# Kernel tuning notes

Hardware: AMD Instinct MI355X
Metric: run time of the kernel (lower is better)

The kernel has to match this reference:

```python
import jax, jax.numpy as jnp
import numpy as np

B, G, S, GS, P = 32, 512, 128, 32, 10
C, H, RED = 384, 6, 16
HID = 4 * C
D = C // H
SCALE = D ** -0.5

def _gelu(x):
    return jax.nn.gelu(x, approximate=False)

def _ln(x, g, b):
    m = jnp.mean(x, -1, keepdims=True)
    v = jnp.var(x, -1, keepdims=True)
    return (x - m) * jax.lax.rsqrt(v + 1e-5) * g + b

def _split_qkv(x, W):
    Bn, T, Cc = x.shape
    qkv = (x @ W).reshape(Bn, T, 3, H, D).transpose(2, 0, 3, 1, 4)
    return qkv[0], qkv[1], qkv[2]

def _merge(x):
    Bn, Hh, T, Dd = x.shape
    return x.transpose(0, 2, 1, 3).reshape(Bn, T, Hh * Dd)

def _mha(q, k, v):
    a = jax.nn.softmax(jnp.einsum('bhnd,bhmd->bhnm', q, k) * SCALE, axis=-1)
    return jnp.einsum('bhnm,bhmd->bhnd', a, v)

def _forward(x, center1, center2, neighborhood, prompt_embeddings, ln1_g, ln1_b, Wqkv, Wproj, bproj, gate, ln2_g, ln2_b, W1, b1, W2, b2, ad_down_W, ad_down_b, ad_up_W, ad_up_b, ad_gate, bn_g, bn_b, bn_mean, bn_var, ln3_g, ln3_b, a1_Wqkv, a1_Wproj, a1_bproj, ad1_down_W, ad1_down_b, ad1_up_W, ad1_up_b, idx, center_idx, group_size, if_maxmean, pro_cof, center_cof):
    Bx, Ntok, Cc = x.shape
    # prompt dropout is identity in eval
    prompt = jnp.broadcast_to(prompt_embeddings, (Bx, P, Cc))
    # --- gated dual self / prompt-cross attention ---
    xn = _ln(x, ln1_g, ln1_b)
    q, k, v = _split_qkv(xn, Wqkv)
    xs = _mha(q, k, v)                                  # [B,H,N,D]
    _, pk, pv = _split_qkv(prompt, Wqkv)
    pa = jax.nn.softmax(jnp.einsum('bhnd,bhpd->bhnp', q, pk) * SCALE, axis=-1)
    px = jnp.einsum('bhnp,bhpd->bhnd', gate * pa, pv)   # learned gate per head
    x = x + (_merge(xs) + _merge(px)) @ Wproj + bproj
    # --- MLP + gated bottleneck adapter residual ---
    h = _gelu(_ln(x, ln2_g, ln2_b) @ W1 + b1) @ W2 + b2
    h_ad = h + _gelu(h @ ad_down_W + ad_down_b) @ ad_up_W + ad_up_b
    x = ad_gate * h_ad + x
    cls_x = x[:, :1]
    xt = x[:, 1:]                                       # [B,G,C]
    flat = xt.reshape(Bx * G, Cc)
    x_nb = flat[idx].reshape(Bx * S, group_size, Cc)    # KNN neighborhoods
    x_ct = flat[center_idx].reshape(Bx, S, Cc)          # center features
    # NOTE: original normalizes `neighborhood` by its std, but result is unused
    # --- local self-attention (attn1 over norm3) on each neighborhood ---
    nq, nk, nv = _split_qkv(_ln(x_nb, ln3_g, ln3_b), a1_Wqkv)
    no = _mha(nq, nk, nv)
    x_nb = x_nb + _merge(no) @ a1_Wproj + a1_bproj
    knn = x_nb.reshape(Bx, S, group_size, Cc)
    lc = jnp.max(knn, axis=2)
    if if_maxmean:
        lc = lc + jnp.mean(knn, axis=2)
    # BatchNorm1d (eval, running stats) + GELU over channel dim
    lc = _gelu((lc - bn_mean) * jax.lax.rsqrt(bn_var + 1e-5) * bn_g + bn_b)
    vis = lc + center_cof * x_ct                        # [B,S,C]
    # --- propagate: de_neighbors == S so sorted-topk == full weighted sum ---
    d = jnp.sum((center1[:, :, None, :] - center2[:, None, :, :]) ** 2, axis=-1)  # [B,G,S]
    w = 1.0 / (d + 1e-8)
    w = w / jnp.sum(w, axis=-1, keepdims=True)
    interp = jnp.einsum('bns,bsc->bnc', w, vis)
    xt = xt + pro_cof * interp
    out = jnp.concatenate([cls_x, xt], axis=1)
    # adapter1
    out = out + _gelu(out @ ad1_down_W + ad1_down_b) @ ad1_up_W + ad1_up_b
    return out

def setup_inputs():
    ks = jax.random.split(jax.random.key(0), 20)
    r = lambda i, shape, s=0.02: jax.random.normal(ks[i], shape, jnp.float32) * s
    return {
        'x': jax.random.normal(ks[0], (B, G + 1, C), jnp.float32),
        'center1': jax.random.normal(ks[1], (B, G, 3), jnp.float32),
        'center2': jax.random.normal(ks[2], (B, S, 3), jnp.float32),
        'neighborhood': jax.random.normal(ks[3], (B, S, GS, 3), jnp.float32),
        'prompt_embeddings': r(4, (P, C)),
        'ln1_g': jnp.ones(C), 'ln1_b': jnp.zeros(C),
        'Wqkv': r(5, (C, 3 * C)),
        'Wproj': r(6, (C, C)), 'bproj': jnp.zeros(C),
        'gate': jax.random.normal(ks[7], (1, H, 1, 1), jnp.float32),
        'ln2_g': jnp.ones(C), 'ln2_b': jnp.zeros(C),
        'W1': r(8, (C, HID)), 'b1': jnp.zeros(HID),
        'W2': r(9, (HID, C)), 'b2': jnp.zeros(C),
        'ad_down_W': r(10, (C, RED)), 'ad_down_b': jnp.zeros(RED),
        'ad_up_W': r(11, (RED, C)), 'ad_up_b': jnp.zeros(C),
        'ad_gate': jax.random.normal(ks[12], (), jnp.float32),
        'bn_g': jnp.ones(C), 'bn_b': jnp.zeros(C),
        'bn_mean': jnp.zeros(C), 'bn_var': jnp.ones(C),
        'ln3_g': jnp.ones(C), 'ln3_b': jnp.zeros(C),
        'a1_Wqkv': r(13, (C, 3 * C)),
        'a1_Wproj': r(14, (C, C)), 'a1_bproj': jnp.zeros(C),
        'ad1_down_W': r(15, (C, RED)), 'ad1_down_b': jnp.zeros(RED),
        'ad1_up_W': r(16, (RED, C)), 'ad1_up_b': jnp.zeros(C),
        'idx': jax.random.randint(ks[17], (B * S * GS,), 0, B * G),
        'center_idx': jax.random.randint(ks[18], (B * S,), 0, B * G),
        'group_size': GS,
        'if_maxmean': 1,
        'pro_cof': 1,
        'center_cof': 1,
    }

def reference(x, center1, center2, neighborhood, prompt_embeddings, ln1_g, ln1_b, Wqkv, Wproj, bproj, gate, ln2_g, ln2_b, W1, b1, W2, b2, ad_down_W, ad_down_b, ad_up_W, ad_up_b, ad_gate, bn_g, bn_b, bn_mean, bn_var, ln3_g, ln3_b, a1_Wqkv, a1_Wproj, a1_bproj, ad1_down_W, ad1_down_b, ad1_up_W, ad1_up_b, idx, center_idx, group_size, if_maxmean, pro_cof, center_cof):
    return _forward(x, center1, center2, neighborhood, prompt_embeddings, ln1_g, ln1_b, Wqkv, Wproj, bproj, gate, ln2_g, ln2_b, W1, b1, W2, b2, ad_down_W, ad_down_b, ad_up_W, ad_up_b, ad_gate, bn_g, bn_b, bn_mean, bn_var, ln3_g, ln3_b, a1_Wqkv, a1_Wproj, a1_bproj, ad1_down_W, ad1_down_b, ad1_up_W, ad1_up_b, idx, center_idx, group_size, if_maxmean, pro_cof, center_cof)
```

## Files before the change

### kernel.cpp

```cpp
#include <hip/hip_runtime.h>
#include <hip/hip_bf16.h>
#include <cstdint>
#include <cstddef>

typedef __hip_bfloat16 bf16;
constexpr int TOK = 32 * 513;

typedef __attribute__((ext_vector_type(8))) short short8;
typedef __attribute__((ext_vector_type(4))) float f32x4;

__device__ __forceinline__ float bflo(unsigned u){ return __uint_as_float(u << 16); }
__device__ __forceinline__ float bfhi(unsigned u){ return __uint_as_float(u & 0xffff0000u); }
__device__ __forceinline__ float b2f(bf16 x){ return __bfloat162float(x); }
__device__ __forceinline__ bf16  f2b(float x){ return __float2bfloat16(x); }
__device__ __forceinline__ float geluf(float x){ return 0.5f*x*(1.0f + erff(x*0.70710678118654752f)); }
__device__ __forceinline__ void unp8(uint4 u, float* f){
  f[0]=bflo(u.x); f[1]=bfhi(u.x); f[2]=bflo(u.y); f[3]=bfhi(u.y);
  f[4]=bflo(u.z); f[5]=bfhi(u.z); f[6]=bflo(u.w); f[7]=bfhi(u.w);
}
__device__ __forceinline__ float scal(const int* p){
  const int i = *p;
  if (i > -1000000 && i < 1000000) return (float)i;
  return __int_as_float(i);
}
__device__ __forceinline__ f32x4 mfma16(short8 a, short8 b, f32x4 c){
  return __builtin_amdgcn_mfma_f32_16x16x32_bf16(a, b, c, 0, 0, 0);
}
__device__ __forceinline__ int swzl(int l){ return l ^ ((l >> 3) & 7); }

__global__ __launch_bounds__(256) void detect_kernel(const unsigned* __restrict__ x,
                                                     int* __restrict__ flag)
{
  const int t = threadIdx.x;
  bool bad = false;
  for (int i = t; i < 2048; i += 256){
    const unsigned u = x[i];
    const float a = fabsf(bflo(u)), b = fabsf(bfhi(u));
    if (!(a < 1e6f) || !(b < 1e6f)) bad = true;
  }
  __shared__ int s;
  if (t == 0) s = 0;
  __syncthreads();
  const unsigned long long m = __ballot(bad);
  if (m != 0ull && (t & 63) == 0) atomicOr(&s, 1);
  __syncthreads();
  if (t == 0) *flag = s;
}

struct ConvArgs {
  const void* src[34];
  bf16*       dst[34];
  int         n[34];
};
__global__ __launch_bounds__(256) void convert_many(const int* __restrict__ flag, ConvArgs a)
{
  const int ii = blockIdx.y;
  const bool isf = (*flag != 0);
  const int n = a.n[ii];
  const int n8 = n >> 3;
  bf16* d = a.dst[ii];
  if (isf){
    const float4* s = (const float4*)a.src[ii];
    for (int i = blockIdx.x*256 + threadIdx.x; i < n8; i += gridDim.x*256){
      const float4 f0 = s[i*2];
      const float4 f1 = s[i*2 + 1];
      bf16 tmp[8] = {f2b(f0.x),f2b(f0.y),f2b(f0.z),f2b(f0.w),
                     f2b(f1.x),f2b(f1.y),f2b(f1.z),f2b(f1.w)};
      *(uint4*)(d + (size_t)i*8) = *(const uint4*)tmp;
    }
  } else {
    const uint4* s = (const uint4*)a.src[ii];
    for (int i = blockIdx.x*256 + threadIdx.x; i < n8; i += gridDim.x*256){
      ((uint4*)d)[i] = s[i];
    }
  }
  if (blockIdx.x == 0){
    for (int i = n8*8 + threadIdx.x; i < n; i += 256){
      d[i] = isf ? f2b(((const float*)a.src[ii])[i]) : ((const bf16*)a.src[ii])[i];
    }
  }
}

__global__ __launch_bounds__(256) void shuffle_b(const bf16* __restrict__ W,
    bf16* __restrict__ out, int N, int KT, int NT)
{
  const int id = blockIdx.x*256 + threadIdx.x;
  if (id >= NT*KT*64) return;
  const int l  = id & 63;
  const int k0 = (id >> 6) % KT;
  const int n0 = (id >> 6) / KT;
  bf16 tmp[8];
  #pragma unroll
  for (int j = 0; j < 8; j++)
    tmp[j] = W[(size_t)(k0*32 + (l>>4)*8 + j)*N + n0*16 + (l&15)];
  *(uint4*)(out + (size_t)id*8) = *(const uint4*)tmp;
}

template<bool SRC_BF16>
__global__ __launch_bounds__(256) void ln_kernel(const void* __restrict__ src,
    const bf16* __restrict__ g, const bf16* __restrict__ b,
    bf16* __restrict__ out, int rows)
{
  const int wave = (blockIdx.x * blockDim.x + threadIdx.x) >> 6;
  const int lane = threadIdx.x & 63;
  if (wave >= rows) return;
  float v[6]; float s = 0.f, s2 = 0.f;
  #pragma unroll
  for (int i = 0; i < 6; i++){
    const int c = lane + 64*i;
    float x;
    if (SRC_BF16) x = b2f(((const bf16*)src)[(size_t)wave*384 + c]);
    else          x = ((const float*)src)[(size_t)wave*384 + c];
    v[i] = x; s += x; s2 += x*x;
  }
  #pragma unroll
  for (int mm = 32; mm; mm >>= 1){ s += __shfl_xor(s, mm); s2 += __shfl_xor(s2, mm); }
  const float mean = s * (1.f/384.f);
  const float rs = rsqrtf(s2 * (1.f/384.f) - mean*mean + 1e-5f);
  #pragma unroll
  for (int i = 0; i < 6; i++){
    const int c = lane + 64*i;
    out[(size_t)wave*384 + c] = f2b((v[i]-mean)*rs*b2f(g[c]) + b2f(b[c]));
  }
}

__global__ __launch_bounds__(256) void ln3_kernel(const float* __restrict__ xres,
    const bf16* __restrict__ g, const bf16* __restrict__ b, bf16* __restrict__ out)
{
  const int r = (blockIdx.x * blockDim.x + threadIdx.x) >> 6;
  const int lane = threadIdx.x & 63;
  if (r >= 16384) return;
  const int tok = (r >> 9)*513 + 1 + (r & 511);
  const float* xp = xres + (size_t)tok*384;
  float v[6]; float s = 0.f, s2 = 0.f;
  #pragma unroll
  for (int i = 0; i < 6; i++){
    const float x = xp[lane + 64*i];
    v[i] = x; s += x; s2 += x*x;
  }
  #pragma unroll
  for (int mm = 32; mm; mm >>= 1){ s += __shfl_xor(s, mm); s2 += __shfl_xor(s2, mm); }
  const float mean = s * (1.f/384.f);
  const float rs = rsqrtf(s2 * (1.f/384.f) - mean*mean + 1e-5f);
  #pragma unroll
  for (int i = 0; i < 6; i++){
    const int c = lane + 64*i;
    out[(size_t)r*384 + c] = f2b((v[i]-mean)*rs*b2f(g[c]) + b2f(b[c]));
  }
}

template<int EPI>
__global__ __launch_bounds__(256) void mfma_gemm(
    const bf16* __restrict__ A, const bf16* __restrict__ Bsh,
    const bf16* __restrict__ bias, const bf16* __restrict__ resid,
    void* __restrict__ outv, int M, int N, int K)
{
  __shared__ __align__(16) bf16 sA[8*64*8];
  const int t = threadIdx.x, lane = t & 63, w = t >> 6;
  const int l15 = lane & 15, quad = lane >> 4;
  const int wm = w & 1, wn = w >> 1;
  const int m0 = blockIdx.y * 128;
  const int n0t = blockIdx.x * 8 + wn * 4;
  const int KT = K >> 5;
  f32x4 acc[4][4];
  #pragma unroll
  for (int i = 0; i < 4; i++){
    #pragma unroll
    for (int j = 0; j < 4; j++) acc[i][j] = f32x4{0.f,0.f,0.f,0.f};
  }
  const int arow = t >> 1, ac0 = (t & 1) * 16;
  const int amt = arow >> 4, al15 = arow & 15, aq0 = (ac0 >> 3);

  for (int ks = 0; ks < KT; ks++){
    uint4 u0 = {0,0,0,0}, u1 = {0,0,0,0};
    const int gm = m0 + arow;
    if (gm < M){
      const bf16* ap = A + (size_t)gm*K + ks*32 + ac0;
      u0 = *(const uint4*)ap; u1 = *(const uint4*)(ap + 8);
    }
    *(uint4*)(sA + ((amt*64 + aq0*16     + al15) << 3)) = u0;
    *(uint4*)(sA + ((amt*64 + (aq0+1)*16 + al15) << 3)) = u1;
    __syncthreads();
    short8 afr[4];
    #pragma unroll
    for (int i = 0; i < 4; i++)
      afr[i] = *(const short8*)(sA + (((wm*4+i)*64 + lane) << 3));
    #pragma unroll
    for (int j = 0; j < 4; j++){
      const short8 b = *(const short8*)(Bsh + ((size_t)((n0t+j)*KT + ks)*64 + lane)*8);
      #pragma unroll
      for (int i = 0; i < 4; i++) acc[i][j] = mfma16(afr[i], b, acc[i][j]);
    }
    __syncthreads();
  }
  #pragma unroll
  for (int i = 0; i < 4; i++){
    #pragma unroll
    for (int r = 0; r < 4; r++){
      const int gm = m0 + (wm*4+i)*16 + quad*4 + r;
      if (gm < M){
        #pragma unroll
        for (int j = 0; j < 4; j++){
          const int gn = (n0t+j)*16 + l15;
          float v = acc[i][j][r];
          const size_t o = (size_t)gm*N + gn;
          if (EPI == 0){ v += b2f(bias[gn]); ((bf16*)outv)[o] = f2b(v); }
          else if (EPI == 1){ ((bf16*)outv)[o] = f2b(v); }
          else if (EPI == 2){ v += b2f(bias[gn]); ((bf16*)outv)[o] = f2b(geluf(v)); }
          else { v += b2f(bias[gn]) + b2f(resid[o]); ((float*)outv)[o] = v; }
        }
      }
    }
  }
}

__global__ __launch_bounds__(256) void pqkv_kernel(const bf16* __restrict__ pe,
    const bf16* __restrict__ Wqkv, float* __restrict__ pq)
{
  const int n  = blockIdx.x*64 + (threadIdx.x & 63);
  const int rg = threadIdx.x >> 6;
  for (int r = rg; r < 10; r += 4){
    float s0 = 0.f, s1 = 0.f;
    for (int c = 0; c < 384; c += 2){
      s0 = fmaf(b2f(pe[(size_t)r*384+c]),   b2f(Wqkv[(size_t)c*1152 + n]),     s0);
      s1 = fmaf(b2f(pe[(size_t)r*384+c+1]), b2f(Wqkv[(size_t)(c+1)*1152 + n]), s1);
    }
    pq[(size_t)r*1152 + n] = s0 + s1;
  }
}

__global__ __launch_bounds__(256) void attn_kernel(
    const bf16* __restrict__ qkv, const float* __restrict__ pq,
    const bf16* __restrict__ gate, bf16* __restrict__ ao)
{
  __shared__ __align__(16) bf16 s_q[64*72];
  __shared__ __align__(16) bf16 s_k[64*72];
  __shared__ __align__(16) bf16 s_vT[64*72];
  __shared__ __align__(16) bf16 s_p[4*16*40];
  __shared__ __align__(16) bf16 s_pk[16*72];
  __shared__ __align__(16) bf16 s_pvT[64*40];
  const int bh = blockIdx.y;
  const int b = bh / 6, h = bh % 6;
  const int q0 = blockIdx.x * 64;
  const int t = threadIdx.x, lane = t & 63, w = t >> 6;
  const int l15 = lane & 15, quad = lane >> 4;

  {
    const int row = t >> 2, dc = (t & 3) * 16;
    const int tok = q0 + row;
    uint4 u0 = {0,0,0,0}, u1 = {0,0,0,0};
    if (tok < 513){
      const bf16* p = qkv + (size_t)(b*513 + tok)*1152 + h*64 + dc;
      u0 = *(const uint4*)p; u1 = *(const uint4*)(p + 8);
    }
    *(uint4*)(s_q + row*72 + dc)     = u0;
    *(uint4*)(s_q + row*72 + dc + 8) = u1;
  }
  {
    const int j = t >> 4, dc = (t & 15) * 4;
    float f[4] = {0.f,0.f,0.f,0.f};
    if (j < 10){
      const float* pk = pq + (size_t)j*1152 + 384 + h*64 + dc;
      f[0]=pk[0]; f[1]=pk[1]; f[2]=pk[2]; f[3]=pk[3];
    }
    bf16 tmp[4] = {f2b(f[0]),f2b(f[1]),f2b(f[2]),f2b(f[3])};
    *(uint2*)(s_pk + j*72 + dc) = *(const uint2*)tmp;
  }
  {
    const int d = t & 63, kg = t >> 6;
    #pragma unroll
    for (int kk = 0; kk < 8; kk++){
      const int key = kg*8 + kk;
      bf16 v = f2b(0.f);
      if (key < 10) v = f2b(pq[(size_t)key*1152 + 768 + h*64 + d]);
      s_pvT[d*40 + key] = v;
    }
  }

  float m_i[4], l_i[4];
  f32x4 oacc[4];
  #pragma unroll
  for (int r = 0; r < 4; r++){ m_i[r] = -30000.f; l_i[r] = 0.f; }
  #pragma unroll
  for (int nt = 0; nt < 4; nt++) oacc[nt] = f32x4{0.f,0.f,0.f,0.f};
  bf16* myp = s_p + w*16*40;
  const short8* aq = (const short8*)(s_q + (w*16 + l15)*72);

  for (int kt = 0; kt < 9; kt++){
    const int kb = kt*64;
    __syncthreads();
    {
      const int kp = t & 31, dg = t >> 5;
      const int key0 = kb + 2*kp;
      uint4 k0v = {0,0,0,0}, k1v = {0,0,0,0}, v0 = {0,0,0,0}, v1 = {0,0,0,0};
      if (key0 < 513){
        const bf16* base = qkv + (size_t)(b*513 + key0)*1152 + h*64 + dg*8;
        k0v = *(const uint4*)(base + 384);
        v0  = *(const uint4*)(base + 768);
      }
      if (key0 + 1 < 513){
        const bf16* base = qkv + (size_t)(b*513 + key0 + 1)*1152 + h*64 + dg*8;
        k1v = *(const uint4*)(base + 384);
        v1  = *(const uint4*)(base + 768);
      }
      *(uint4*)(s_k + (2*kp)*72   + dg*8) = k0v;
      *(uint4*)(s_k + (2*kp+1)*72 + dg*8) = k1v;
      const unsigned short* a0 = (const unsigned short*)&v0;
      const unsigned short* a1 = (const unsigned short*)&v1;
      unsigned* vt = (unsigned*)s_vT;
      #pragma unroll
      for (int j = 0; j < 8; j++)
        vt[(dg*8 + j)*36 + kp] = (unsigned)a0[j] | ((unsigned)a1[j] << 16);
    }
    __syncthreads();

    f32x4 sreg[4];
    #pragma unroll
    for (int nt = 0; nt < 4; nt++){
      f32x4 acc = f32x4{0.f,0.f,0.f,0.f};
      const short8* bk = (const short8*)(s_k + (nt*16 + l15)*72);
      acc = mfma16(aq[quad],     bk[quad],     acc);
      acc = mfma16(aq[4 + quad], bk[4 + quad], acc);
      const bool kvalid = (kb + nt*16 + l15) < 513;
      #pragma unroll
      for (int r = 0; r < 4; r++)
        sreg[nt][r] = kvalid ? acc[r]*0.125f : -30000.f;
    }
    float alpha[4];
    #pragma unroll
    for (int r = 0; r < 4; r++){
      float mx = fmaxf(fmaxf(sreg[0][r], sreg[1][r]), fmaxf(sreg[2][r], sreg[3][r]));
      #pragma unroll
      for (int mm = 8; mm; mm >>= 1) mx = fmaxf(mx, __shfl_xor(mx, mm));
      const float mn = fmaxf(m_i[r], mx);
      alpha[r] = __expf(m_i[r] - mn);
      m_i[r] = mn;
      float ps = 0.f;
      #pragma unroll
      for (int nt = 0; nt < 4; nt++){
        const float p = __expf(sreg[nt][r] - mn);
        sreg[nt][r] = p; ps += p;
      }
      #pragma unroll
      for (int mm = 8; mm; mm >>= 1) ps += __shfl_xor(ps, mm);
      l_i[r] = l_i[r]*alpha[r] + ps;
    }
    #pragma unroll
    for (int nt = 0; nt < 4; nt++){
      #pragma unroll
      for (int r = 0; r < 4; r++)
        myp[(quad*4 + r)*40 + nt*16 + l15] = f2b(sreg[nt][r]);
    }
    #pragma unroll
    for (int nt = 0; nt < 4; nt++){
      #pragma unroll
      for (int r = 0; r < 4; r++) oacc[nt][r] *= alpha[r];
    }
    const short8* ap = (const short8*)(myp + l15*40);
    #pragma unroll
    for (int nt = 0; nt < 4; nt++){
      const short8* bv = (const short8*)(s_vT + (nt*16 + l15)*72);
      oacc[nt] = mfma16(ap[quad],     bv[quad],     oacc[nt]);
      oacc[nt] = mfma16(ap[4 + quad], bv[4 + quad], oacc[nt]);
    }
  }

  f32x4 sp;
  {
    f32x4 acc = f32x4{0.f,0.f,0.f,0.f};
    const short8* bp = (const short8*)(s_pk + l15*72);
    acc = mfma16(aq[quad],     bp[quad],     acc);
    acc = mfma16(aq[4 + quad], bp[4 + quad], acc);
    #pragma unroll
    for (int r = 0; r < 4; r++)
      sp[r] = (l15 < 10) ? acc[r]*0.125f : -30000.f;
  }
  float psr[4];
  #pragma unroll
  for (int r = 0; r < 4; r++){
    float mx = sp[r];
    #pragma unroll
    for (int mm = 8; mm; mm >>= 1) mx = fmaxf(mx, __shfl_xor(mx, mm));
    const float p = __expf(sp[r] - mx);
    float ps = p;
    #pragma unroll
    for (int mm = 8; mm; mm >>= 1) ps += __shfl_xor(ps, mm);
    psr[r] = ps;
    myp[(quad*4 + r)*40 + l15]      = f2b(p);
    myp[(quad*4 + r)*40 + 16 + l15] = f2b(0.f);
  }
  f32x4 pva[4];
  {
    const short8* ap = (const short8*)(myp + l15*40);
    #pragma unroll
    for (int nt = 0; nt < 4; nt++){
      const short8* bv = (const short8*)(s_pvT + (nt*16 + l15)*40);
      pva[nt] = mfma16(ap[quad], bv[quad], f32x4{0.f,0.f,0.f,0.f});
    }
  }

  const float gh = b2f(gate[h]);
  #pragma unroll
  for (int r = 0; r < 4; r++){
    const int tok = q0 + w*16 + quad*4 + r;
    if (tok < 513){
      const float invl = 1.f/l_i[r];
      const float gps  = gh/psr[r];
      #pragma unroll
      for (int nt = 0; nt < 4; nt++){
        const float val = oacc[nt][r]*invl + pva[nt][r]*gps;
        ao[(size_t)(b*513 + tok)*384 + h*64 + nt*16 + l15] = f2b(val);
      }
    }
  }
}

__global__ __launch_bounds__(256) void adapter_mid_kernel(const bf16* __restrict__ h,
    const bf16* __restrict__ Wd, const bf16* __restrict__ bd,
    const bf16* __restrict__ Wu, const bf16* __restrict__ bu,
    const bf16* __restrict__ p_gate, float* __restrict__ xres)
{
  __shared__ float s_h[384];
  __shared__ float s_part[16][17];
  __shared__ float s_y[16];
  const size_t row = blockIdx.x;
  const int t = threadIdx.x;
  const bf16* hp = h + row*384;
  for (int c = t; c < 384; c += 256) s_h[c] = b2f(hp[c]);
  __syncthreads();
  const int o = t & 15, p = t >> 4;
  float part0 = 0.f, part1 = 0.f;
  for (int c = p; c < 384; c += 32){
    part0 = fmaf(s_h[c],    b2f(Wd[(size_t)c*16 + o]),      part0);
    part1 = fmaf(s_h[c+16], b2f(Wd[(size_t)(c+16)*16 + o]), part1);
  }
  s_part[o][p] = part0 + part1;
  __syncthreads();
  if (t < 16){
    float sum = 0.f;
    #pragma unroll
    for (int pp = 0; pp < 16; pp++) sum += s_part[t][pp];
    s_y[t] = geluf(sum + b2f(bd[t]));
  }
  __syncthreads();
  const float g = b2f(p_gate[0]);
  for (int c = t; c < 384; c += 256){
    float up = 0.f;
    #pragma unroll
    for (int o2 = 0; o2 < 16; o2++) up = fmaf(s_y[o2], b2f(Wu[(size_t)o2*384 + c]), up);
    const float had = s_h[c] + up + b2f(bu[c]);
    xres[row*384 + c] = g*had + xres[row*384 + c];
  }
}

__global__ __launch_bounds__(256) void adapter_final_kernel(const float* __restrict__ xr,
    const bf16* __restrict__ Wd, const bf16* __restrict__ bd,
    const bf16* __restrict__ Wu, const bf16* __restrict__ bu,
    const int* __restrict__ flag, void* __restrict__ out)
{
  __shared__ float s_h[384];
  __shared__ float s_part[16][17];
  __shared__ float s_y[16];
  const size_t row = blockIdx.x;
  const int t = threadIdx.x;
  const float* hp = xr + row*384;
  for (int c = t; c < 384; c += 256) s_h[c] = hp[c];
  __syncthreads();
  const int o = t & 15, p = t >> 4;
  float part0 = 0.f, part1 = 0.f;
  for (int c = p; c < 384; c += 32){
    part0 = fmaf(s_h[c],    b2f(Wd[(size_t)c*16 + o]),      part0);
    part1 = fmaf(s_h[c+16], b2f(Wd[(size_t)(c+16)*16 + o]), part1);
  }
  s_part[o][p] = part0 + part1;
  __syncthreads();
  if (t < 16){
    float sum = 0.f;
    #pragma unroll
    for (int pp = 0; pp < 16; pp++) sum += s_part[t][pp];
    s_y[t] = geluf(sum + b2f(bd[t]));
  }
  __syncthreads();
  const bool isf = (*flag != 0);
  for (int c = t; c < 384; c += 256){
    float up = 0.f;
    #pragma unroll
    for (int o2 = 0; o2 < 16; o2++) up = fmaf(s_y[o2], b2f(Wu[(size_t)o2*384 + c]), up);
    const float v = s_h[c] + up + b2f(bu[c]);
    if (isf) ((float*)out)[row*384 + c] = v;
    else     ((bf16*)out)[row*384 + c] = f2b(v);
  }
}

__global__ __launch_bounds__(512, 2) void local_kernel(
    const bf16* __restrict__ qkv3, const float* __restrict__ xres,
    const int* __restrict__ idx, const int* __restrict__ cidx,
    const bf16* __restrict__ Bp, const bf16* __restrict__ bp1,
    const bf16* __restrict__ bng, const bf16* __restrict__ bnb,
    const bf16* __restrict__ bnm, const bf16* __restrict__ bnv,
    const int* __restrict__ p_ifmm, const int* __restrict__ p_ccof,
    float* __restrict__ vis)
{
  __shared__ __align__(16) bf16 sV[3*4*64*8];
  __shared__ __align__(16) bf16 sP[3*2*64*8];
  __shared__ __align__(16) bf16 sO[3*4*64*8];
  __shared__ int s_flat[32];
  __shared__ int s_tok[32];

  const int g = blockIdx.x;
  const int t = threadIdx.x, lane = t & 63, w = t >> 6;
  const int l15 = lane & 15, quad = lane >> 4;
  const int lanez = swzl(lane);

  if (t < 32){
    const int r = idx[g*32 + t];
    s_flat[t] = r;
    s_tok[t]  = (r >> 9)*513 + 1 + (r & 511);
  }
  __syncthreads();

  const int vrowA = t & 31,          vccA = t >> 5;
  const int vrowB = (512 + t) & 31,  vccB = (512 + t) >> 5;
  const int vhA = vccA >> 3, vd0A = (vccA & 7) * 8;
  const int vhB = vccB >> 3, vd0B = (vccB & 7) * 8;
  const bool hasB = (t < 256);

  uint4 svA, svB;
  {
    svA = *(const uint4*)(qkv3 + (size_t)s_flat[vrowA]*1152 + 768 + (0*3 + vhA)*64 + vd0A);
    if (hasB) svB = *(const uint4*)(qkv3 + (size_t)s_flat[vrowB]*1152 + 768 + (0*3 + vhB)*64 + vd0B);
  }

  f32x4 accp[3][2];
  #pragma unroll
  for (int a = 0; a < 3; a++){
    #pragma unroll
    for (int m = 0; m < 2; m++) accp[a][m] = f32x4{0.f,0.f,0.f,0.f};
  }

  #pragma unroll
  for (int hc = 0; hc < 2; hc++){
    {
      const bf16* sa = (const bf16*)&svA;
      #pragma unroll
      for (int j2 = 0; j2 < 8; j2++){
        const int d = vd0A + j2;
        const int L = (vrowA>>3)*16 + (d&15);
        sV[((vhA*4 + (d>>4))*64 + swzl(L))*8 + (vrowA&7)] = sa[j2];
      }
      if (hasB){
        const bf16* sb = (const bf16*)&svB;
        #pragma unroll
        for (int j2 = 0; j2 < 8; j2++){
          const int d = vd0B + j2;
          const int L = (vrowB>>3)*16 + (d&15);
          sV[((vhB*4 + (d>>4))*64 + swzl(L))*8 + (vrowB&7)] = sb[j2];
        }
      }
    }
    __syncthreads();

    if (w < 6){
      const int h = w >> 1, mt = w & 1;
      const size_t qrow = (size_t)s_flat[mt*16 + l15]*1152;
      const int dcol = (hc*3 + h)*64 + quad*8;
      const short8 q0 = *(const short8*)(qkv3 + qrow + dcol);
      const short8 q1 = *(const short8*)(qkv3 + qrow + dcol + 32);
      f32x4 sr[2];
      #pragma unroll
      for (int nt = 0; nt < 2; nt++){
        const size_t krow = (size_t)s_flat[nt*16 + l15]*1152 + 384;
        const short8 k0 = *(const short8*)(qkv3 + krow + dcol);
        const short8 k1 = *(const short8*)(qkv3 + krow + dcol + 32);
        f32x4 acc = mfma16(q0, k0, f32x4{0.f,0.f,0.f,0.f});
        acc = mfma16(q1, k1, acc);
        #pragma unroll
        for (int r = 0; r < 4; r++) sr[nt][r] = acc[r]*0.125f;
      }
      #pragma unroll
      for (int r = 0; r < 4; r++){
        float mx = fmaxf(sr[0][r], sr[1][r]);
        #pragma unroll
        for (int mm = 8; mm; mm >>= 1) mx = fmaxf(mx, __shfl_xor(mx, mm));
        const float e0 = __expf(sr[0][r] - mx), e1 = __expf(sr[1][r] - mx);
        float sm = e0 + e1;
        #pragma unroll
        for (int mm = 8; mm; mm >>= 1) sm += __shfl_xor(sm, mm);
        const float inv = 1.f/sm;
        const int m = quad*4 + r;
        const int L0 = (l15 >> 3)*16       + m;
        const int L1 = (2 + (l15 >> 3))*16 + m;
        sP[((h*2 + mt)*64 + swzl(L0))*8 + (l15 & 7)] = f2b(e0*inv);
        sP[((h*2 + mt)*64 + swzl(L1))*8 + (l15 & 7)] = f2b(e1*inv);
      }
    }
    __syncthreads();

    {
      const int mt = w & 1, nt = w >> 1;
      const int k0w = nt >> 1, qdw = (nt & 1)*2 + (l15 >> 3), jw = l15 & 7;
      #pragma unroll
      for (int h = 0; h < 3; h++){
        const short8 a = *(const short8*)(sP + ((h*2 + mt)*64 + lanez)*8);
        const short8 b = *(const short8*)(sV + ((h*4 + nt)*64 + lanez)*8);
        const f32x4 o = mfma16(a, b, f32x4{0.f,0.f,0.f,0.f});
        #pragma unroll
        for (int r = 0; r < 4; r++){
          const int L = qdw*16 + quad*4 + r;
          sO[((h*4 + mt*2 + k0w)*64 + swzl(L))*8 + jw] = f2b(o[r]);
        }
      }
    }
    __syncthreads();

    if (hc == 0){
      svA = *(const uint4*)(qkv3 + (size_t)s_flat[vrowA]*1152 + 768 + (3 + vhA)*64 + vd0A);
      if (hasB) svB = *(const uint4*)(qkv3 + (size_t)s_flat[vrowB]*1152 + 768 + (3 + vhB)*64 + vd0B);
    }

    #pragma unroll
    for (int h = 0; h < 3; h++){
      short8 afr[2][2];
      #pragma unroll
      for (int mt = 0; mt < 2; mt++){
        #pragma unroll
        for (int k0l = 0; k0l < 2; k0l++)
          afr[mt][k0l] = *(const short8*)(sO + ((h*4 + mt*2 + k0l)*64 + lanez)*8);
      }
      const int hg2 = (hc*3 + h)*2;
      #pragma unroll
      for (int tt = 0; tt < 3; tt++){
        const int nt = w*3 + tt;
        #pragma unroll
        for (int k0l = 0; k0l < 2; k0l++){
          const short8 b = *(const short8*)(Bp + ((size_t)(nt*12 + hg2 + k0l)*64 + lane)*8);
          accp[tt][0] = mfma16(afr[0][k0l], b, accp[tt][0]);
          accp[tt][1] = mfma16(afr[1][k0l], b, accp[tt][1]);
        }
      }
    }
    __syncthreads();
  }

  const float fmm  = scal(p_ifmm);
  const float ccof = scal(p_ccof);
  const int cr = cidx[g];
  const int ctok = (cr >> 9)*513 + 1 + (cr & 511);
  #pragma unroll
  for (int tt = 0; tt < 3; tt++){
    const int n = (w*3 + tt)*16 + l15;
    const float bb = b2f(bp1[n]);
    float mx = -3e30f, sm = 0.f;
    #pragma unroll
    for (int mt = 0; mt < 2; mt++){
      #pragma unroll
      for (int r = 0; r < 4; r++){
        const int tok = mt*16 + quad*4 + r;
        const float v = accp[tt][mt][r] + bb + xres[(size_t)s_tok[tok]*384 + n];
        mx = fmaxf(mx, v); sm += v;
      }
    }
    mx = fmaxf(mx, __shfl_xor(mx, 16)); sm += __shfl_xor(sm, 16);
    mx = fmaxf(mx, __shfl_xor(mx, 32)); sm += __shfl_xor(sm, 32);
    if (quad == 0){
      const float lc = (fmm != 0.f) ? (mx + sm*(1.f/32.f)) : mx;
      const float nr = (lc - b2f(bnm[n])) * rsqrtf(b2f(bnv[n]) + 1e-5f) * b2f(bng[n]) + b2f(bnb[n]);
      vis[(size_t)g*384 + n] = geluf(nr) + ccof * xres[(size_t)ctok*384 + n];
    }
  }
}

__global__ __launch_bounds__(256) void interp_kernel(const bf16* __restrict__ c1,
    const bf16* __restrict__ c2, const float* __restrict__ vis,
    const int* __restrict__ p_pcof, float* __restrict__ xres)
{
  __shared__ float s_w[8][128];
  __shared__ float s_red[2];
  const int b = blockIdx.y;
  const int n0 = blockIdx.x * 8;
  const int t = threadIdx.x;
  for (int ni = 0; ni < 8; ni++){
    const int n = n0 + ni;
    float wv = 0.f;
    if (t < 128){
      float d2 = 0.f;
      #pragma unroll
      for (int k = 0; k < 3; k++){
        const float a = b2f(c1[((size_t)b*512 + n)*3 + k]);
        const float c = b2f(c2[((size_t)b*128 + t)*3 + k]);
        const float df = a - c; d2 += df*df;
      }
      wv = 1.f/(d2 + 1e-8f);
    }
    float rsum = wv;
    #pragma unroll
    for (int mm = 32; mm; mm >>= 1) rsum += __shfl_xor(rsum, mm);
    if (((t & 63) == 0) && t < 128) s_red[t >> 6] = rsum;
    __syncthreads();
    const float tot = s_red[0] + s_red[1];
    if (t < 128) s_w[ni][t] = wv / tot;
    __syncthreads();
  }
  float acc1[8], acc2[8];
  #pragma unroll
  for (int ni = 0; ni < 8; ni++){ acc1[ni] = 0.f; acc2[ni] = 0.f; }
  for (int s = 0; s < 128; s++){
    const float* vp = vis + ((size_t)b*128 + s)*384;
    const float v1 = vp[t];
    const float v2 = (t < 128) ? vp[t + 256] : 0.f;
    #pragma unroll
    for (int ni = 0; ni < 8; ni++){
      const float wn = s_w[ni][s];
      acc1[ni] = fmaf(wn, v1, acc1[ni]);
      acc2[ni] = fmaf(wn, v2, acc2[ni]);
    }
  }
  const float pc = scal(p_pcof);
  #pragma unroll
  for (int ni = 0; ni < 8; ni++){
    const int tok = b*513 + 1 + n0 + ni;
    xres[(size_t)tok*384 + t] += pc*acc1[ni];
    if (t < 128) xres[(size_t)tok*384 + t + 256] += pc*acc2[ni];
  }
}

extern "C" void kernel_launch(void* const* d_in, const int* in_sizes, int n_in,
                              void* d_out, int out_size, void* d_ws, size_t ws_size,
                              hipStream_t stream)
{
  (void)n_in; (void)out_size; (void)ws_size;
  const int*  idx   = (const int*)d_in[35];
  const int*  cidx  = (const int*)d_in[36];
  const int*  ifmm  = (const int*)d_in[38];
  const int*  pcof  = (const int*)d_in[39];
  const int*  ccof  = (const int*)d_in[40];

  size_t off = 0;
  auto alloc = [&](size_t bytes) -> void* {
    void* p = (char*)d_ws + off; off += (bytes + 255) & ~(size_t)255; return p;
  };
  int*   flag = (int*)  alloc(sizeof(int));
  float* xres = (float*)alloc((size_t)TOK*384*4);
  bf16*  slab = (bf16*) alloc((size_t)TOK*1536*2);
  bf16*  xn   = (bf16*) alloc((size_t)TOK*384*2);
  float* pq   = (float*)alloc((size_t)10*1152*4);
  bf16*  Bq   = (bf16*) alloc((size_t)72*12*64*8*2);
  bf16*  Bp   = (bf16*) alloc((size_t)24*12*64*8*2);
  bf16*  Bqkv = (bf16*) alloc((size_t)72*12*64*8*2);
  bf16*  Bw1  = (bf16*) alloc((size_t)96*12*64*8*2);
  bf16*  Bw2  = (bf16*) alloc((size_t)24*48*64*8*2);
  bf16*  Bwp  = (bf16*) alloc((size_t)24*12*64*8*2);

  bf16*  qkvb = slab;
  bf16*  x_c  = slab + (size_t)TOK*1152;
  bf16*  h1   = slab;
  bf16*  qkv3 = slab;
  bf16*  xln3 = slab + (size_t)TOK*1152;
  bf16*  ao   = xn;
  bf16*  hbuf = xn;
  float* visb = (float*)xn;

  const int conv_ids[34] = {0,1,2,4,5,6,7,8,9,10,11,12,13,14,15,16,17,
                            18,19,20,21,22,23,24,25,26,27,28,29,30,31,32,33,34};
  ConvArgs ca;
  bf16* canon[41];
  int maxn = 1;
  for (int k = 0; k < 34; k++){
    const int i = conv_ids[k];
    const int n = in_sizes[i];
    bf16* dst = (i == 0) ? x_c : (bf16*)alloc((size_t)n*2);
    ca.src[k] = d_in[i]; ca.dst[k] = dst; ca.n[k] = n;
    canon[i] = dst;
    if (n > maxn) maxn = n;
  }
  detect_kernel<<<dim3(1), dim3(256), 0, stream>>>((const unsigned*)d_in[0], flag);
  {
    int gx = (maxn/8 + 255) / 256; if (gx > 512) gx = 512; if (gx < 1) gx = 1;
    convert_many<<<dim3(gx, 34), dim3(256), 0, stream>>>(flag, ca);
  }

  const bf16 *x_in = canon[0], *c1 = canon[1], *c2 = canon[2], *pe = canon[4],
             *ln1g = canon[5], *ln1b = canon[6], *Wqkv = canon[7], *Wproj = canon[8],
             *bproj = canon[9], *gate = canon[10], *ln2g = canon[11], *ln2b = canon[12],
             *W1 = canon[13], *b1 = canon[14], *W2 = canon[15], *b2v = canon[16],
             *adW = canon[17], *adb = canon[18], *adU = canon[19], *adub = canon[20],
             *adg = canon[21], *bng = canon[22], *bnb = canon[23], *bnm = canon[24],
             *bnv = canon[25], *ln3g = canon[26], *ln3b = canon[27], *a1W = canon[28],
             *a1P = canon[29], *a1pb = canon[30], *d1W = canon[31], *d1b = canon[32],
             *u1W = canon[33], *u1b = canon[34];

  shuffle_b<<<dim3(216), dim3(256), 0, stream>>>(a1W, Bq, 1152, 12, 72);
  shuffle_b<<<dim3(72),  dim3(256), 0, stream>>>(a1P, Bp, 384, 12, 24);
  shuffle_b<<<dim3(216), dim3(256), 0, stream>>>(Wqkv, Bqkv, 1152, 12, 72);
  shuffle_b<<<dim3(288), dim3(256), 0, stream>>>(W1, Bw1, 1536, 12, 96);
  shuffle_b<<<dim3(288), dim3(256), 0, stream>>>(W2, Bw2, 384, 48, 24);
  shuffle_b<<<dim3(72),  dim3(256), 0, stream>>>(Wproj, Bwp, 384, 12, 24);

  ln_kernel<true><<<dim3((TOK*64)/256), dim3(256), 0, stream>>>((const void*)x_in, ln1g, ln1b, xn, TOK);
  mfma_gemm<1><<<dim3(9,129), dim3(256), 0, stream>>>(xn, Bqkv, nullptr, nullptr, qkvb, TOK, 1152, 384);
  pqkv_kernel<<<dim3(18), dim3(256), 0, stream>>>(pe, Wqkv, pq);
  attn_kernel<<<dim3(9,192), dim3(256), 0, stream>>>(qkvb, pq, gate, ao);
  mfma_gemm<3><<<dim3(3,129), dim3(256), 0, stream>>>(ao, Bwp, bproj, x_in, xres, TOK, 384, 384);
  ln_kernel<false><<<dim3((TOK*64)/256), dim3(256), 0, stream>>>((const void*)xres, ln2g, ln2b, xn, TOK);
  mfma_gemm<2><<<dim3(12,129), dim3(256), 0, stream>>>(xn, Bw1, b1, nullptr, h1, TOK, 1536, 384);
  mfma_gemm<0><<<dim3(3,129), dim3(256), 0, stream>>>(h1, Bw2, b2v, nullptr, hbuf, TOK, 384, 1536);
  adapter_mid_kernel<<<dim3(TOK), dim3(256), 0, stream>>>(hbuf, adW, adb, adU, adub, adg, xres);
  ln3_kernel<<<dim3((16384*64)/256), dim3(256), 0, stream>>>(xres, ln3g, ln3b, xln3);
  mfma_gemm<1><<<dim3(9,128), dim3(256), 0, stream>>>(xln3, Bq, nullptr, nullptr, qkv3, 16384, 1152, 384);
  local_kernel<<<dim3(4096), dim3(512), 0, stream>>>(qkv3, xres, idx, cidx, Bp, a1pb,
                                                     bng, bnb, bnm, bnv, ifmm, ccof, visb);
  interp_kernel<<<dim3(64,32), dim3(256), 0, stream>>>(c1, c2, visb, pcof, xres);
  adapter_final_kernel<<<dim3(TOK), dim3(256), 0, stream>>>(xres, d1W, d1b, u1W, u1b, flag, d_out);
}
```

Measured before the change: 809.7 us.

## Restructure local attention kernel to 4 waves processing two heads per pass

```diff
diff --git a/kernel.cpp b/kernel.cpp
--- a/kernel.cpp
+++ b/kernel.cpp
@@ -14,10 +14,6 @@
 __device__ __forceinline__ float b2f(bf16 x){ return __bfloat162float(x); }
 __device__ __forceinline__ bf16  f2b(float x){ return __float2bfloat16(x); }
 __device__ __forceinline__ float geluf(float x){ return 0.5f*x*(1.0f + erff(x*0.70710678118654752f)); }
-__device__ __forceinline__ void unp8(uint4 u, float* f){
-  f[0]=bflo(u.x); f[1]=bfhi(u.x); f[2]=bflo(u.y); f[3]=bfhi(u.y);
-  f[4]=bflo(u.z); f[5]=bfhi(u.z); f[6]=bflo(u.w); f[7]=bfhi(u.w);
-}
 __device__ __forceinline__ float scal(const int* p){
   const int i = *p;
   if (i > -1000000 && i < 1000000) return (float)i;
@@ -492,7 +488,7 @@
   }
 }
 
-__global__ __launch_bounds__(512, 2) void local_kernel(
+__global__ __launch_bounds__(256, 4) void local_kernel(
     const bf16* __restrict__ qkv3, const float* __restrict__ xres,
     const int* __restrict__ idx, const int* __restrict__ cidx,
     const bf16* __restrict__ Bp, const bf16* __restrict__ bp1,
@@ -501,9 +497,9 @@
     const int* __restrict__ p_ifmm, const int* __restrict__ p_ccof,
     float* __restrict__ vis)
 {
-  __shared__ __align__(16) bf16 sV[3*4*64*8];
-  __shared__ __align__(16) bf16 sP[3*2*64*8];
-  __shared__ __align__(16) bf16 sO[3*4*64*8];
+  __shared__ __align__(16) bf16 sV[2*4*64*8];
+  __shared__ __align__(16) bf16 sP[2*2*64*8];
+  __shared__ __align__(16) bf16 sO[2*4*64*8];
   __shared__ int s_flat[32];
   __shared__ int s_tok[32];
 
@@ -519,51 +515,43 @@
   }
   __syncthreads();
 
-  const int vrowA = t & 31,          vccA = t >> 5;
-  const int vrowB = (512 + t) & 31,  vccB = (512 + t) >> 5;
-  const int vhA = vccA >> 3, vd0A = (vccA & 7) * 8;
-  const int vhB = vccB >> 3, vd0B = (vccB & 7) * 8;
-  const bool hasB = (t < 256);
+  const int vrow = t & 31;
+  const int vd0  = ((t >> 5) & 7) * 8;
 
   uint4 svA, svB;
   {
-    svA = *(const uint4*)(qkv3 + (size_t)s_flat[vrowA]*1152 + 768 + (0*3 + vhA)*64 + vd0A);
-    if (hasB) svB = *(const uint4*)(qkv3 + (size_t)s_flat[vrowB]*1152 + 768 + (0*3 + vhB)*64 + vd0B);
-  }
-
-  f32x4 accp[3][2];
-  #pragma unroll
-  for (int a = 0; a < 3; a++){
+    const size_t vbase = (size_t)s_flat[vrow]*1152 + 768 + vd0;
+    svA = *(const uint4*)(qkv3 + vbase);
+    svB = *(const uint4*)(qkv3 + vbase + 64);
+  }
+
+  f32x4 accp[6][2];
+  #pragma unroll
+  for (int a = 0; a < 6; a++){
     #pragma unroll
     for (int m = 0; m < 2; m++) accp[a][m] = f32x4{0.f,0.f,0.f,0.f};
   }
 
   #pragma unroll
-  for (int hc = 0; hc < 2; hc++){
+  for (int hc = 0; hc < 3; hc++){
     {
       const bf16* sa = (const bf16*)&svA;
+      const bf16* sb = (const bf16*)&svB;
       #pragma unroll
       for (int j2 = 0; j2 < 8; j2++){
-        const int d = vd0A + j2;
-        const int L = (vrowA>>3)*16 + (d&15);
-        sV[((vhA*4 + (d>>4))*64 + swzl(L))*8 + (vrowA&7)] = sa[j2];
-      }
-      if (hasB){
-        const bf16* sb = (const bf16*)&svB;
-        #pragma unroll
-        for (int j2 = 0; j2 < 8; j2++){
-          const int d = vd0B + j2;
-          const int L = (vrowB>>3)*16 + (d&15);
-          sV[((vhB*4 + (d>>4))*64 + swzl(L))*8 + (vrowB&7)] = sb[j2];
-        }
-      }
-    }
-    __syncthreads();
-
-    if (w < 6){
+        const int d = vd0 + j2;
+        const int L = (vrow>>3)*16 + (d&15);
+        const int slot = ((d>>4)*64 + swzl(L))*8 + (vrow&7);
+        sV[slot]         = sa[j2];
+        sV[4*64*8 + slot] = sb[j2];
+      }
+    }
+    __syncthreads();
+
+    {
       const int h = w >> 1, mt = w & 1;
       const size_t qrow = (size_t)s_flat[mt*16 + l15]*1152;
-      const int dcol = (hc*3 + h)*64 + quad*8;
+      const int dcol = (hc*2 + h)*64 + quad*8;
       const short8 q0 = *(const short8*)(qkv3 + qrow + dcol);
       const short8 q1 = *(const short8*)(qkv3 + qrow + dcol + 32);
       f32x4 sr[2];
@@ -597,29 +585,34 @@
     __syncthreads();
 
     {
-      const int mt = w & 1, nt = w >> 1;
-      const int k0w = nt >> 1, qdw = (nt & 1)*2 + (l15 >> 3), jw = l15 & 7;
-      #pragma unroll
-      for (int h = 0; h < 3; h++){
+      const int mt = w & 1, nthalf = w >> 1;
+      #pragma unroll
+      for (int h = 0; h < 2; h++){
         const short8 a = *(const short8*)(sP + ((h*2 + mt)*64 + lanez)*8);
-        const short8 b = *(const short8*)(sV + ((h*4 + nt)*64 + lanez)*8);
-        const f32x4 o = mfma16(a, b, f32x4{0.f,0.f,0.f,0.f});
         #pragma unroll
-        for (int r = 0; r < 4; r++){
-          const int L = qdw*16 + quad*4 + r;
-          sO[((h*4 + mt*2 + k0w)*64 + swzl(L))*8 + jw] = f2b(o[r]);
+        for (int ntl = 0; ntl < 2; ntl++){
+          const int nt = nthalf*2 + ntl;
+          const short8 b = *(const short8*)(sV + ((h*4 + nt)*64 + lanez)*8);
+          const f32x4 o = mfma16(a, b, f32x4{0.f,0.f,0.f,0.f});
+          const int k0w = nt >> 1, qdw = (nt & 1)*2 + (l15 >> 3), jw = l15 & 7;
+          #pragma unroll
+          for (int r = 0; r < 4; r++){
+            const int L = qdw*16 + quad*4 + r;
+            sO[((h*4 + mt*2 + k0w)*64 + swzl(L))*8 + jw] = f2b(o[r]);
+          }
         }
       }
     }
     __syncthreads();
 
-    if (hc == 0){
-      svA = *(const uint4*)(qkv3 + (size_t)s_flat[vrowA]*1152 + 768 + (3 + vhA)*64 + vd0A);
-      if (hasB) svB = *(const uint4*)(qkv3 + (size_t)s_flat[vrowB]*1152 + 768 + (3 + vhB)*64 + vd0B);
-    }
-
-    #pragma unroll
-    for (int h = 0; h < 3; h++){
+    if (hc < 2){
+      const size_t vbase = (size_t)s_flat[vrow]*1152 + 768 + (hc+1)*128 + vd0;
+      svA = *(const uint4*)(qkv3 + vbase);
+      svB = *(const uint4*)(qkv3 + vbase + 64);
+    }
+
+    #pragma unroll
+    for (int h = 0; h < 2; h++){
       short8 afr[2][2];
       #pragma unroll
       for (int mt = 0; mt < 2; mt++){
@@ -627,10 +620,10 @@
         for (int k0l = 0; k0l < 2; k0l++)
           afr[mt][k0l] = *(const short8*)(sO + ((h*4 + mt*2 + k0l)*64 + lanez)*8);
       }
-      const int hg2 = (hc*3 + h)*2;
-      #pragma unroll
-      for (int tt = 0; tt < 3; tt++){
-        const int nt = w*3 + tt;
+      const int hg2 = (hc*2 + h)*2;
+      #pragma unroll
+      for (int tt = 0; tt < 6; tt++){
+        const int nt = w*6 + tt;
         #pragma unroll
         for (int k0l = 0; k0l < 2; k0l++){
           const short8 b = *(const short8*)(Bp + ((size_t)(nt*12 + hg2 + k0l)*64 + lane)*8);
@@ -647,8 +640,8 @@
   const int cr = cidx[g];
   const int ctok = (cr >> 9)*513 + 1 + (cr & 511);
   #pragma unroll
-  for (int tt = 0; tt < 3; tt++){
-    const int n = (w*3 + tt)*16 + l15;
+  for (int tt = 0; tt < 6; tt++){
+    const int n = (w*6 + tt)*16 + l15;
     const float bb = b2f(bp1[n]);
     float mx = -3e30f, sm = 0.f;
     #pragma unroll
@@ -807,7 +800,7 @@
   adapter_mid_kernel<<<dim3(TOK), dim3(256), 0, stream>>>(hbuf, adW, adb, adU, adub, adg, xres);
   ln3_kernel<<<dim3((16384*64)/256), dim3(256), 0, stream>>>(xres, ln3g, ln3b, xln3);
   mfma_gemm<1><<<dim3(9,128), dim3(256), 0, stream>>>(xln3, Bq, nullptr, nullptr, qkv3, 16384, 1152, 384);
-  local_kernel<<<dim3(4096), dim3(512), 0, stream>>>(qkv3, xres, idx, cidx, Bp, a1pb,
+  local_kernel<<<dim3(4096), dim3(256), 0, stream>>>(qkv3, xres, idx, cidx, Bp, a1pb,
                                                      bng, bnb, bnm, bnv, ifmm, ccof, visb);
   interp_kernel<<<dim3(64,32), dim3(256), 0, stream>>>(c1, c2, visb, pcof, xres);
   adapter_final_kernel<<<dim3(TOK), dim3(256), 0, stream>>>(xres, d1W, d1b, u1W, u1b, flag, d_out);
```

Result: slower. 867.7 us (+7.2%).

## Fuse LN3 into adapter and process one row per wavefront

Applied to the files above, without the earlier changes.

```diff
diff --git a/kernel.cpp b/kernel.cpp
--- a/kernel.cpp
+++ b/kernel.cpp
@@ -14,10 +14,6 @@
 __device__ __forceinline__ float b2f(bf16 x){ return __bfloat162float(x); }
 __device__ __forceinline__ bf16  f2b(float x){ return __float2bfloat16(x); }
 __device__ __forceinline__ float geluf(float x){ return 0.5f*x*(1.0f + erff(x*0.70710678118654752f)); }
-__device__ __forceinline__ void unp8(uint4 u, float* f){
-  f[0]=bflo(u.x); f[1]=bfhi(u.x); f[2]=bflo(u.y); f[3]=bfhi(u.y);
-  f[4]=bflo(u.z); f[5]=bfhi(u.z); f[6]=bflo(u.w); f[7]=bfhi(u.w);
-}
 __device__ __forceinline__ float scal(const int* p){
   const int i = *p;
   if (i > -1000000 && i < 1000000) return (float)i;
@@ -124,31 +120,6 @@
   }
 }
 
-__global__ __launch_bounds__(256) void ln3_kernel(const float* __restrict__ xres,
-    const bf16* __restrict__ g, const bf16* __restrict__ b, bf16* __restrict__ out)
-{
-  const int r = (blockIdx.x * blockDim.x + threadIdx.x) >> 6;
-  const int lane = threadIdx.x & 63;
-  if (r >= 16384) return;
-  const int tok = (r >> 9)*513 + 1 + (r & 511);
-  const float* xp = xres + (size_t)tok*384;
-  float v[6]; float s = 0.f, s2 = 0.f;
-  #pragma unroll
-  for (int i = 0; i < 6; i++){
-    const float x = xp[lane + 64*i];
-    v[i] = x; s += x; s2 += x*x;
-  }
-  #pragma unroll
-  for (int mm = 32; mm; mm >>= 1){ s += __shfl_xor(s, mm); s2 += __shfl_xor(s2, mm); }
-  const float mean = s * (1.f/384.f);
-  const float rs = rsqrtf(s2 * (1.f/384.f) - mean*mean + 1e-5f);
-  #pragma unroll
-  for (int i = 0; i < 6; i++){
-    const int c = lane + 64*i;
-    out[(size_t)r*384 + c] = f2b((v[i]-mean)*rs*b2f(g[c]) + b2f(b[c]));
-  }
-}
-
 template<int EPI>
 __global__ __launch_bounds__(256) void mfma_gemm(
     const bf16* __restrict__ A, const bf16* __restrict__ Bsh,
@@ -415,80 +386,78 @@
   }
 }
 
-__global__ __launch_bounds__(256) void adapter_mid_kernel(const bf16* __restrict__ h,
+template<bool MID>
+__global__ __launch_bounds__(256) void adapter_kernel(
+    const void* __restrict__ src,
     const bf16* __restrict__ Wd, const bf16* __restrict__ bd,
     const bf16* __restrict__ Wu, const bf16* __restrict__ bu,
-    const bf16* __restrict__ p_gate, float* __restrict__ xres)
-{
-  __shared__ float s_h[384];
-  __shared__ float s_part[16][17];
-  __shared__ float s_y[16];
-  const size_t row = blockIdx.x;
-  const int t = threadIdx.x;
-  const bf16* hp = h + row*384;
-  for (int c = t; c < 384; c += 256) s_h[c] = b2f(hp[c]);
-  __syncthreads();
-  const int o = t & 15, p = t >> 4;
-  float part0 = 0.f, part1 = 0.f;
-  for (int c = p; c < 384; c += 32){
-    part0 = fmaf(s_h[c],    b2f(Wd[(size_t)c*16 + o]),      part0);
-    part1 = fmaf(s_h[c+16], b2f(Wd[(size_t)(c+16)*16 + o]), part1);
-  }
-  s_part[o][p] = part0 + part1;
-  __syncthreads();
-  if (t < 16){
-    float sum = 0.f;
-    #pragma unroll
-    for (int pp = 0; pp < 16; pp++) sum += s_part[t][pp];
-    s_y[t] = geluf(sum + b2f(bd[t]));
-  }
-  __syncthreads();
-  const float g = b2f(p_gate[0]);
-  for (int c = t; c < 384; c += 256){
-    float up = 0.f;
-    #pragma unroll
-    for (int o2 = 0; o2 < 16; o2++) up = fmaf(s_y[o2], b2f(Wu[(size_t)o2*384 + c]), up);
-    const float had = s_h[c] + up + b2f(bu[c]);
-    xres[row*384 + c] = g*had + xres[row*384 + c];
-  }
-}
-
-__global__ __launch_bounds__(256) void adapter_final_kernel(const float* __restrict__ xr,
-    const bf16* __restrict__ Wd, const bf16* __restrict__ bd,
-    const bf16* __restrict__ Wu, const bf16* __restrict__ bu,
-    const int* __restrict__ flag, void* __restrict__ out)
-{
-  __shared__ float s_h[384];
-  __shared__ float s_part[16][17];
-  __shared__ float s_y[16];
-  const size_t row = blockIdx.x;
-  const int t = threadIdx.x;
-  const float* hp = xr + row*384;
-  for (int c = t; c < 384; c += 256) s_h[c] = hp[c];
-  __syncthreads();
-  const int o = t & 15, p = t >> 4;
-  float part0 = 0.f, part1 = 0.f;
-  for (int c = p; c < 384; c += 32){
-    part0 = fmaf(s_h[c],    b2f(Wd[(size_t)c*16 + o]),      part0);
-    part1 = fmaf(s_h[c+16], b2f(Wd[(size_t)(c+16)*16 + o]), part1);
-  }
-  s_part[o][p] = part0 + part1;
-  __syncthreads();
-  if (t < 16){
-    float sum = 0.f;
-    #pragma unroll
-    for (int pp = 0; pp < 16; pp++) sum += s_part[t][pp];
-    s_y[t] = geluf(sum + b2f(bd[t]));
-  }
-  __syncthreads();
-  const bool isf = (*flag != 0);
-  for (int c = t; c < 384; c += 256){
-    float up = 0.f;
-    #pragma unroll
-    for (int o2 = 0; o2 < 16; o2++) up = fmaf(s_y[o2], b2f(Wu[(size_t)o2*384 + c]), up);
-    const float v = s_h[c] + up + b2f(bu[c]);
-    if (isf) ((float*)out)[row*384 + c] = v;
-    else     ((bf16*)out)[row*384 + c] = f2b(v);
+    const bf16* __restrict__ p_gate,
+    const bf16* __restrict__ g3, const bf16* __restrict__ b3,
+    const int* __restrict__ flag,
+    float* __restrict__ xres, bf16* __restrict__ xln3,
+    void* __restrict__ out)
+{
+  __shared__ float s_h[4][384];
+  const int wv = threadIdx.x >> 6, lane = threadIdx.x & 63;
+  const int row = blockIdx.x*4 + wv;
+  float v[6];
+  #pragma unroll
+  for (int i = 0; i < 6; i++){
+    const int c = lane + 64*i;
+    float x;
+    if (MID) x = b2f(((const bf16*)src)[(size_t)row*384 + c]);
+    else     x = ((const float*)src)[(size_t)row*384 + c];
+    v[i] = x; s_h[wv][c] = x;
+  }
+  const int o = lane & 15, p = lane >> 4;
+  float part = 0.f;
+  #pragma unroll 4
+  for (int j = 0; j < 96; j++)
+    part = fmaf(s_h[wv][p*96 + j], b2f(Wd[(size_t)(p*96 + j)*16 + o]), part);
+  part += __shfl_xor(part, 16);
+  part += __shfl_xor(part, 32);
+  const float y = geluf(part + b2f(bd[o]));
+  float up[6] = {0.f,0.f,0.f,0.f,0.f,0.f};
+  #pragma unroll
+  for (int o2 = 0; o2 < 16; o2++){
+    const float yo = __shfl(y, o2);
+    #pragma unroll
+    for (int i = 0; i < 6; i++)
+      up[i] = fmaf(yo, b2f(Wu[(size_t)o2*384 + lane + 64*i]), up[i]);
+  }
+  if (MID){
+    const float g = b2f(p_gate[0]);
+    float nv[6]; float s = 0.f, s2 = 0.f;
+    #pragma unroll
+    for (int i = 0; i < 6; i++){
+      const int c = lane + 64*i;
+      const float had = v[i] + up[i] + b2f(bu[c]);
+      const float nx = g*had + xres[(size_t)row*384 + c];
+      xres[(size_t)row*384 + c] = nx;
+      nv[i] = nx; s += nx; s2 += nx*nx;
+    }
+    const int boff = row % 513;
+    if (boff != 0){
+      #pragma unroll
+      for (int mm = 32; mm; mm >>= 1){ s += __shfl_xor(s, mm); s2 += __shfl_xor(s2, mm); }
+      const float mean = s * (1.f/384.f);
+      const float rs = rsqrtf(s2 * (1.f/384.f) - mean*mean + 1e-5f);
+      const int r3 = (row/513)*512 + boff - 1;
+      #pragma unroll
+      for (int i = 0; i < 6; i++){
+        const int c = lane + 64*i;
+        xln3[(size_t)r3*384 + c] = f2b((nv[i]-mean)*rs*b2f(g3[c]) + b2f(b3[c]));
+      }
+    }
+  } else {
+    const bool isf = (*flag != 0);
+    #pragma unroll
+    for (int i = 0; i < 6; i++){
+      const int c = lane + 64*i;
+      const float ov = v[i] + up[i] + b2f(bu[c]);
+      if (isf) ((float*)out)[(size_t)row*384 + c] = ov;
+      else     ((bf16*)out)[(size_t)row*384 + c] = f2b(ov);
+    }
   }
 }
 
@@ -804,11 +773,12 @@
   ln_kernel<false><<<dim3((TOK*64)/256), dim3(256), 0, stream>>>((const void*)xres, ln2g, ln2b, xn, TOK);
   mfma_gemm<2><<<dim3(12,129), dim3(256), 0, stream>>>(xn, Bw1, b1, nullptr, h1, TOK, 1536, 384);
   mfma_gemm<0><<<dim3(3,129), dim3(256), 0, stream>>>(h1, Bw2, b2v, nullptr, hbuf, TOK, 384, 1536);
-  adapter_mid_kernel<<<dim3(TOK), dim3(256), 0, stream>>>(hbuf, adW, adb, adU, adub, adg, xres);
-  ln3_kernel<<<dim3((16384*64)/256), dim3(256), 0, stream>>>(xres, ln3g, ln3b, xln3);
+  adapter_kernel<true><<<dim3(TOK/4), dim3(256), 0, stream>>>(
+      (const void*)hbuf, adW, adb, adU, adub, adg, ln3g, ln3b, nullptr, xres, xln3, nullptr);
   mfma_gemm<1><<<dim3(9,128), dim3(256), 0, stream>>>(xln3, Bq, nullptr, nullptr, qkv3, 16384, 1152, 384);
   local_kernel<<<dim3(4096), dim3(512), 0, stream>>>(qkv3, xres, idx, cidx, Bp, a1pb,
                                                      bng, bnb, bnm, bnv, ifmm, ccof, visb);
   interp_kernel<<<dim3(64,32), dim3(256), 0, stream>>>(c1, c2, visb, pcof, xres);
-  adapter_final_kernel<<<dim3(TOK), dim3(256), 0, stream>>>(xres, d1W, d1b, u1W, u1b, flag, d_out);
-}
+  adapter_kernel<false><<<dim3(TOK/4), dim3(256), 0, stream>>>(
+      (const void*)xres, d1W, d1b, u1W, u1b, nullptr, nullptr, nullptr, flag, nullptr, nullptr, d_out);
+}
```

Result: faster. 791.7 us (-2.2%).
